# Kernel optimization log

Hardware: AMD Instinct MI355X
Metric: run time of the kernel (lower is better)

## Reference

```python
import jax, jax.numpy as jnp
import numpy as np

B, C, W, H, D = 4, 32, 64, 64, 64


def setup_inputs() -> dict:
    key = jax.random.key(0)
    ks = jax.random.split(key, 8)
    x = jax.random.normal(ks[0], (B, C, W, H, D), dtype=jnp.float32)
    # 1x1x1 Conv3d == per-voxel channel mixing: weight (C_out, C_in), bias (C_out,)
    Wq = jax.random.normal(ks[1], (C, C), dtype=jnp.float32) * 0.05
    bq = jax.random.normal(ks[2], (C,), dtype=jnp.float32) * 0.05
    Wk = jax.random.normal(ks[3], (C, C), dtype=jnp.float32) * 0.05
    bk = jax.random.normal(ks[4], (C,), dtype=jnp.float32) * 0.05
    Wv = jax.random.normal(ks[5], (C, C), dtype=jnp.float32) * 0.05
    bv = jax.random.normal(ks[6], (C,), dtype=jnp.float32) * 0.05
    gamma = jnp.float32(0.1)  # torch inits to 0; nonzero so output depends on attention
    return {"x": x, "Wq": Wq, "bq": bq, "Wk": Wk, "bk": bk, "Wv": Wv, "bv": bv, "gamma": gamma}


def reference(x, Wq, bq, Wk, bk, Wv, bv, gamma):
    b, c, w, h, d = x.shape
    N = w * h * d

    def proj(Wt, bt):
        # 1x1x1 conv then torch's .view(b, -1, c): a raw row-major reshape of
        # (b, c, w, h, d) -> (b, N, c) that interleaves channel/spatial (faithful).
        y = jnp.einsum('oc,bcwhd->bowhd', Wt, x) + bt[None, :, None, None, None]
        return y.reshape(b, N, c)

    q = proj(Wq, bq)  # (b, N, c)
    k = proj(Wk, bk)
    v = proj(Wv, bv)
    s = jnp.einsum('bnc,bnd->bcd', q, k)          # q^T k: tiny (b, c, c)
    a = jax.nn.softmax(s, axis=-1)
    scores = jnp.einsum('bnc,bcd->bnd', v, a)     # (b, N, c)
    return x + gamma * scores.reshape(b, c, w, h, d)
```

## Files before the change

### kernel.cpp

```cpp
#include <hip/hip_runtime.h>

typedef __attribute__((ext_vector_type(8))) short bf16x8;
typedef __attribute__((ext_vector_type(4))) float f32x4;

#define MSP   262144
#define BATCH 4
#define TPOS  256
#define NT1   4
#define NBLK1 (MSP / TPOS / NT1)
#define NBLK2 (MSP / TPOS)

#define OFF_U      0
#define OFF_V      32
#define OFF_BETA   64
#define OFF_CA     96
#define OFF_P      256
#define OFF_CS     4352
#define OFF_UFRAG  8448
#define OFF_WVFRAG 9472
#define OFF_AFRAG  9984

#define GLDS16(gsrc, ldst)                                               \
  __builtin_amdgcn_global_load_lds(                                      \
      (const __attribute__((address_space(1))) unsigned int*)(gsrc),     \
      (__attribute__((address_space(3))) unsigned int*)(ldst), 16, 0, 0)

__device__ __forceinline__ unsigned short f2bf(float f) {
  unsigned int u = __float_as_uint(f);
  u += 0x7fffu + ((u >> 16) & 1u);
  return (unsigned short)(u >> 16);
}
__device__ __forceinline__ float bf2f(unsigned short h) {
  return __uint_as_float(((unsigned int)h) << 16);
}
__device__ __forceinline__ void split2(float f, short* hi, short* lo) {
  unsigned int u = __float_as_uint(f);
  unsigned int uh = u + (0x7fffu + ((u >> 16) & 1u));
  *hi = (short)(uh >> 16);
  const float r = f - __uint_as_float(uh & 0xffff0000u);
  *lo = (short)(__float_as_uint(r) >> 16);
}

#define MFMA(A, B, C) __builtin_amdgcn_mfma_f32_16x16x32_bf16(A, B, C, 0, 0, 0)


__global__ __launch_bounds__(1024) void prep_kernel(
    const float* __restrict__ Wq, const float* __restrict__ bq,
    const float* __restrict__ Wk, const float* __restrict__ bk,
    const float* __restrict__ Wv, float* __restrict__ ws) {
  __shared__ float Ulds[32][32];
  const int tid = threadIdx.x;
  const int aa = tid & 31, bb = tid >> 5;
  float s = 0.f;
  for (int ch = 0; ch < 32; ++ch) s = fmaf(Wq[ch * 32 + aa], Wk[ch * 32 + bb], s);
  Ulds[aa][bb] = s;
  if (tid < 32) {
    float u = 0.f, v = 0.f;
    for (int ch = 0; ch < 32; ++ch) {
      u = fmaf(Wq[ch * 32 + tid], bk[ch], u);
      v = fmaf(bq[ch], Wk[ch * 32 + tid], v);
    }
    ws[OFF_U + tid] = u;
    ws[OFF_V + tid] = v;
  }
  if (tid == 0) {
    float bt = 0.f;
    for (int ch = 0; ch < 32; ++ch) bt = fmaf(bq[ch], bk[ch], bt);
    ws[OFF_BETA] = bt;
  }
  for (int k = tid; k < 8192; k += 1024) ws[OFF_P + k] = 0.f;
  __syncthreads();
  if (tid < 64) {
    const int lm = tid & 15, lb = tid >> 4;
    unsigned short* ufr = (unsigned short*)(ws + OFF_UFRAG);
    unsigned short* wfr = (unsigned short*)(ws + OFF_WVFRAG);
#pragma unroll
    for (int ct = 0; ct < 2; ++ct) {
#pragma unroll
      for (int r = 0; r < 8; ++r) {
        const int kk = (r < 4) ? lb * 4 + r : 16 + lb * 4 + (r - 4);
        const float uval = Ulds[ct * 16 + lm][kk];
        const unsigned short h = f2bf(uval);
        ufr[((ct * 2 + 0) * 64 + tid) * 8 + r] = h;
        ufr[((ct * 2 + 1) * 64 + tid) * 8 + r] = f2bf(uval - bf2f(h));
        wfr[(ct * 64 + tid) * 8 + r] = f2bf(Wv[(ct * 16 + lm) * 32 + kk]);
      }
    }
  }
}

__global__ __launch_bounds__(256) void pass1_kernel(const float* __restrict__ x,
                                                    float* __restrict__ ws) {
  __shared__ float XT[8192];
  const int tid = threadIdx.x;
  const int w = tid >> 6, l = tid & 63, lm = tid & 15, lb = (tid >> 4) & 3;
  const int b = blockIdx.y;
  const size_t xbase = (size_t)b * 32 * MSP;

  const bf16x8* UF = (const bf16x8*)(ws + OFF_UFRAG);
  const bf16x8 uh0 = UF[0 * 64 + l];
  const bf16x8 ul0 = UF[1 * 64 + l];
  const bf16x8 uh1 = UF[2 * 64 + l];
  const bf16x8 ul1 = UF[3 * 64 + l];

  int ldsoff[8];
#pragma unroll
  for (int r = 0; r < 8; ++r) {
    const int ch = (r < 4) ? lb * 4 + r : 16 + lb * 4 + (r - 4);
    ldsoff[r] = ch * 256 + lm;
  }
  const float* rowsrc[8];
#pragma unroll
  for (int rr = 0; rr < 8; ++rr)
    rowsrc[rr] = x + xbase + (size_t)(w * 8 + rr) * MSP + l * 4;

  f32x4 p00 = {0, 0, 0, 0}, p01 = {0, 0, 0, 0}, p10 = {0, 0, 0, 0}, p11 = {0, 0, 0, 0};
  float cs0[8], cs1[8];
#pragma unroll
  for (int r = 0; r < 8; ++r) { cs0[r] = 0.f; cs1[r] = 0.f; }

  const int tile0 = blockIdx.x * NT1;
#pragma unroll 1
  for (int t = 0; t < NT1; ++t) {
    const int pos0 = (tile0 + t) * TPOS;
    __syncthreads();
#pragma unroll
    for (int rr = 0; rr < 8; ++rr)
      GLDS16(rowsrc[rr] + pos0, &XT[(w * 8 + rr) * 256]);
    __syncthreads();

#pragma unroll
    for (int g2 = 0; g2 < 2; ++g2) {
      const int pl = (w * 2 + g2) * 32;
      float xf0[8], xf1[8];
#pragma unroll
      for (int r = 0; r < 8; ++r) {
        xf0[r] = XT[ldsoff[r] + pl];
        xf1[r] = XT[ldsoff[r] + pl + 16];
      }
      bf16x8 xh0, xl0, xh1, xl1;
#pragma unroll
      for (int r = 0; r < 8; ++r) {
        short h, lo;
        split2(xf0[r], &h, &lo); xh0[r] = h; xl0[r] = lo;
        split2(xf1[r], &h, &lo); xh1[r] = h; xl1[r] = lo;
        cs0[r] += xf0[r];  cs1[r] += xf1[r];
      }

      f32x4 y00 = {0,0,0,0}, y01 = {0,0,0,0}, y10 = {0,0,0,0}, y11 = {0,0,0,0};
      y00 = MFMA(uh0, xh0, y00); y00 = MFMA(uh0, xl0, y00); y00 = MFMA(ul0, xh0, y00);
      y01 = MFMA(uh1, xh0, y01); y01 = MFMA(uh1, xl0, y01); y01 = MFMA(ul1, xh0, y01);
      y10 = MFMA(uh0, xh1, y10); y10 = MFMA(uh0, xl1, y10); y10 = MFMA(ul0, xh1, y10);
      y11 = MFMA(uh1, xh1, y11); y11 = MFMA(uh1, xl1, y11); y11 = MFMA(ul1, xh1, y11);

      bf16x8 yh0, yl0, yh1, yl1;
#pragma unroll
      for (int r = 0; r < 4; ++r) {
        short h, lo;
        split2(y00[r], &h, &lo); yh0[r] = h; yl0[r] = lo;
        split2(y10[r], &h, &lo); yh1[r] = h; yl1[r] = lo;
      }
#pragma unroll
      for (int r = 4; r < 8; ++r) {
        short h, lo;
        split2(y01[r - 4], &h, &lo); yh0[r] = h; yl0[r] = lo;
        split2(y11[r - 4], &h, &lo); yh1[r] = h; yl1[r] = lo;
      }

      p00 = MFMA(xh0, yh0, p00); p00 = MFMA(xh0, yl0, p00); p00 = MFMA(xl0, yh0, p00);
      p01 = MFMA(xh0, yh1, p01); p01 = MFMA(xh0, yl1, p01); p01 = MFMA(xl0, yh1, p01);
      p10 = MFMA(xh1, yh0, p10); p10 = MFMA(xh1, yl0, p10); p10 = MFMA(xl1, yh0, p10);
      p11 = MFMA(xh1, yh1, p11); p11 = MFMA(xh1, yl1, p11); p11 = MFMA(xl1, yh1, p11);
    }
  }

  __syncthreads();
  float* red = XT;
#pragma unroll
  for (int r = 0; r < 4; ++r) {
    red[w * 1024 + (lb * 4 + r) * 32 + lm]           = p00[r];
    red[w * 1024 + (lb * 4 + r) * 32 + 16 + lm]      = p01[r];
    red[w * 1024 + (16 + lb * 4 + r) * 32 + lm]      = p10[r];
    red[w * 1024 + (16 + lb * 4 + r) * 32 + 16 + lm] = p11[r];
  }
  __syncthreads();
  for (int k = tid; k < 1024; k += 256) {
    const float s = red[k] + red[1024 + k] + red[2048 + k] + red[3072 + k];
    atomicAdd(&ws[OFF_P + b * 1024 + k], s);
  }
  __syncthreads();
#pragma unroll
  for (int r = 0; r < 8; ++r) {
    const int ch = (r < 4) ? lb * 4 + r : 16 + lb * 4 + (r - 4);
    red[w * 1024 + ch * 32 + lm]      = cs0[r];
    red[w * 1024 + ch * 32 + 16 + lm] = cs1[r];
  }
  __syncthreads();
  for (int k = tid; k < 1024; k += 256) {
    const float s = red[k] + red[1024 + k] + red[2048 + k] + red[3072 + k];
    atomicAdd(&ws[OFF_CS + b * 1024 + k], s);
  }
}

__global__ __launch_bounds__(1024) void softmax_kernel(float* __restrict__ ws) {
  const int j = threadIdx.x, i = threadIdx.y, b = blockIdx.x;
  __shared__ float A_lds[32][32];
  float s = ws[OFF_P + (b * 32 + i) * 32 + j] + 8192.0f * ws[OFF_BETA];
  for (int a = 0; a < 32; ++a) {
    s = fmaf(ws[OFF_U + a], ws[OFF_CS + (b * 32 + a) * 32 + i], s);
    s = fmaf(ws[OFF_V + a], ws[OFF_CS + (b * 32 + a) * 32 + j], s);
  }
  float mx = s;
#pragma unroll
  for (int off = 16; off > 0; off >>= 1) mx = fmaxf(mx, __shfl_xor(mx, off, 32));
  const float e = expf(s - mx);
  float sum = e;
#pragma unroll
  for (int off = 16; off > 0; off >>= 1) sum += __shfl_xor(sum, off, 32);
  A_lds[i][j] = e / sum;
  __syncthreads();
  if (i == 0) {
    float c = 0.f;
    for (int ii = 0; ii < 32; ++ii) c += A_lds[ii][j];
    ws[OFF_CA + b * 32 + j] = c;
  }
  const int tid = i * 32 + j;
  if (tid < 64) {
    const int lm = tid & 15, lb = tid >> 4;
    unsigned short* afr = (unsigned short*)(ws + OFF_AFRAG);
#pragma unroll
    for (int mt = 0; mt < 2; ++mt) {
#pragma unroll
      for (int r = 0; r < 8; ++r) {
        const int kk = (r < 4) ? lb * 4 + r : 16 + lb * 4 + (r - 4);
        afr[((b * 2 + mt) * 64 + tid) * 8 + r] = f2bf(A_lds[kk][mt * 16 + lm]);
      }
    }
  }
}

__global__ __launch_bounds__(256) void pass2_kernel(
    const float* __restrict__ x, const float* __restrict__ bv,
    const float* __restrict__ gm, const float* __restrict__ ws,
    float* __restrict__ out) {
  __shared__ float XT[8192];
  const int tid = threadIdx.x;
  const int w = tid >> 6, l = tid & 63, lm = tid & 15, lb = (tid >> 4) & 3;
  const int b = blockIdx.y;
  const size_t xbase = (size_t)b * 32 * MSP;
  const int pos0 = blockIdx.x * TPOS;

#pragma unroll
  for (int rr = 0; rr < 8; ++rr) {
    const int row = w * 8 + rr;
    const int csrc = ((l + rr) & 63) << 2;
    GLDS16(x + xbase + (size_t)row * MSP + pos0 + csrc, &XT[row * 256]);
  }

  const bf16x8* WF = (const bf16x8*)(ws + OFF_WVFRAG);
  const bf16x8 wv0 = WF[0 * 64 + l];
  const bf16x8 wv1 = WF[1 * 64 + l];
  const bf16x8* AF = (const bf16x8*)(ws + OFF_AFRAG);
  const bf16x8 a0 = AF[(b * 2 + 0) * 64 + l];
  const bf16x8 a1 = AF[(b * 2 + 1) * 64 + l];
  const float gamma = gm[0];
  const float bv0 = bv[lm], bv1 = bv[16 + lm];

  float i00[4], i01[4], i10[4], i11[4];
#pragma unroll
  for (int r = 0; r < 4; ++r) {
    const float c0 = ws[OFF_CA + b * 32 + lb * 4 + r];
    const float c1 = ws[OFF_CA + b * 32 + 16 + lb * 4 + r];
    i00[r] = bv0 * c0; i01[r] = bv1 * c0;
    i10[r] = bv0 * c1; i11[r] = bv1 * c1;
  }

  const int c3 = lm & 3, q = lm >> 2;
  int fbase[8], dr[8];
#pragma unroll
  for (int r = 0; r < 8; ++r) {
    const int ch = (r < 4) ? lb * 4 + r : 16 + lb * 4 + (r - 4);
    fbase[r] = ch * 256 + c3;
    dr[r] = q - (ch & 7);
  }
  const int dres = lb - (lm & 7);
  __syncthreads();

#pragma unroll
  for (int g2 = 0; g2 < 2; ++g2) {
    const int pl4 = (w * 2 + g2) * 8;
    bf16x8 xh0, xh1;
#pragma unroll
    for (int r = 0; r < 8; ++r) {
      const int f0 = fbase[r] + (((pl4 + dr[r]) & 63) << 2);
      const int f1 = fbase[r] + (((pl4 + 4 + dr[r]) & 63) << 2);
      xh0[r] = (short)f2bf(XT[f0]);
      xh1[r] = (short)f2bf(XT[f1]);
    }
    f32x4 v00 = {0,0,0,0}, v01 = {0,0,0,0}, v10 = {0,0,0,0}, v11 = {0,0,0,0};
    v00 = MFMA(xh0, wv0, v00); v01 = MFMA(xh0, wv1, v01);
    v10 = MFMA(xh1, wv0, v10); v11 = MFMA(xh1, wv1, v11);

    bf16x8 vb0, vb1;
#pragma unroll
    for (int r = 0; r < 4; ++r) { vb0[r] = (short)f2bf(v00[r]); vb1[r] = (short)f2bf(v01[r]); }
#pragma unroll
    for (int r = 4; r < 8; ++r) { vb0[r] = (short)f2bf(v10[r - 4]); vb1[r] = (short)f2bf(v11[r - 4]); }

    f32x4 t00 = {i00[0], i00[1], i00[2], i00[3]};
    f32x4 t01 = {i01[0], i01[1], i01[2], i01[3]};
    f32x4 t10 = {i10[0], i10[1], i10[2], i10[3]};
    f32x4 t11 = {i11[0], i11[1], i11[2], i11[3]};
    t00 = MFMA(a0, vb0, t00); t01 = MFMA(a0, vb1, t01);
    t10 = MFMA(a1, vb0, t10); t11 = MFMA(a1, vb1, t11);

    const int p0g = pos0 + (pl4 << 2);
#define EPI(TT, MT, CT)                                                           \
    {                                                                             \
      const int F = ((CT) * 16 + lm) * 256 +                                      \
                    (((pl4 + (MT) * 4 + dres) & 63) << 2);                        \
      const f32x4 xr = *reinterpret_cast<const f32x4*>(&XT[F]);                   \
      const size_t addr = xbase + (size_t)((CT) * 16 + lm) * MSP +                \
                          (size_t)(p0g + (MT) * 16 + lb * 4);                     \
      f32x4 o;                                                                    \
      o[0] = fmaf(gamma, TT[0], xr[0]); o[1] = fmaf(gamma, TT[1], xr[1]);         \
      o[2] = fmaf(gamma, TT[2], xr[2]); o[3] = fmaf(gamma, TT[3], xr[3]);         \
      *reinterpret_cast<f32x4*>(out + addr) = o;                                  \
    }
    EPI(t00, 0, 0); EPI(t01, 0, 1); EPI(t10, 1, 0); EPI(t11, 1, 1);
#undef EPI
  }
}

extern "C" void kernel_launch(void* const* d_in, const int* in_sizes, int n_in,
                              void* d_out, int out_size, void* d_ws, size_t ws_size,
                              hipStream_t stream) {
  const float* x  = (const float*)d_in[0];
  const float* Wq = (const float*)d_in[1];
  const float* bq = (const float*)d_in[2];
  const float* Wk = (const float*)d_in[3];
  const float* bk = (const float*)d_in[4];
  const float* Wv = (const float*)d_in[5];
  const float* bv = (const float*)d_in[6];
  const float* gm = (const float*)d_in[7];
  float* out = (float*)d_out;
  float* ws  = (float*)d_ws;

  prep_kernel<<<1, 1024, 0, stream>>>(Wq, bq, Wk, bk, Wv, ws);
  pass1_kernel<<<dim3(NBLK1, BATCH), 256, 0, stream>>>(x, ws);
  softmax_kernel<<<BATCH, dim3(32, 32), 0, stream>>>(ws);
  pass2_kernel<<<dim3(NBLK2, BATCH), 256, 0, stream>>>(x, bv, gm, ws, out);
}
```

Measured before the change: 97.59 us.

## Fold prep and softmax into passes, double-buffer tile loads, larger per-block tiles

Removes the separate prep and softmax kernels. Each pass1 block now computes Wq^T Wk in LDS, and each pass2 block redundantly recomputes the softmax and bias terms from the workspace sums, with zeroing done by a memset. Both passes now process 8 tiles per block with double-buffered global-to-LDS loads so the next tile's fetch overlaps compute. pass1 pads LDS rows to 258 floats, presumably to reduce bank conflicts. The trade is fewer launches and better latency hiding against redundant per-block setup work, larger LDS use, and fewer blocks in pass2.

Measured after the change: 83.81 us. 1.16x faster.

```diff
diff --git a/kernel.cpp b/kernel.cpp
--- a/kernel.cpp
+++ b/kernel.cpp
@@ -6,19 +6,14 @@
 #define MSP   262144
 #define BATCH 4
 #define TPOS  256
-#define NT1   4
-#define NBLK1 (MSP / TPOS / NT1)
-#define NBLK2 (MSP / TPOS)
-
-#define OFF_U      0
-#define OFF_V      32
-#define OFF_BETA   64
-#define OFF_CA     96
-#define OFF_P      256
-#define OFF_CS     4352
-#define OFF_UFRAG  8448
-#define OFF_WVFRAG 9472
-#define OFF_AFRAG  9984
+#define NT    8
+#define NBLK  (MSP / TPOS / NT)
+
+#define LROW1 258
+#define TSZ1  (32 * LROW1)
+
+#define OFF_P  0
+#define OFF_CS 4096
 
 #define GLDS16(gsrc, ldst)                                               \
   __builtin_amdgcn_global_load_lds(                                      \
@@ -29,9 +24,6 @@
   unsigned int u = __float_as_uint(f);
   u += 0x7fffu + ((u >> 16) & 1u);
   return (unsigned short)(u >> 16);
-}
-__device__ __forceinline__ float bf2f(unsigned short h) {
-  return __uint_as_float(((unsigned int)h) << 16);
 }
 __device__ __forceinline__ void split2(float f, short* hi, short* lo) {
   unsigned int u = __float_as_uint(f);
@@ -44,90 +36,76 @@
 #define MFMA(A, B, C) __builtin_amdgcn_mfma_f32_16x16x32_bf16(A, B, C, 0, 0, 0)
 
 
-__global__ __launch_bounds__(1024) void prep_kernel(
-    const float* __restrict__ Wq, const float* __restrict__ bq,
-    const float* __restrict__ Wk, const float* __restrict__ bk,
-    const float* __restrict__ Wv, float* __restrict__ ws) {
-  __shared__ float Ulds[32][32];
-  const int tid = threadIdx.x;
-  const int aa = tid & 31, bb = tid >> 5;
-  float s = 0.f;
-  for (int ch = 0; ch < 32; ++ch) s = fmaf(Wq[ch * 32 + aa], Wk[ch * 32 + bb], s);
-  Ulds[aa][bb] = s;
-  if (tid < 32) {
-    float u = 0.f, v = 0.f;
-    for (int ch = 0; ch < 32; ++ch) {
-      u = fmaf(Wq[ch * 32 + tid], bk[ch], u);
-      v = fmaf(bq[ch], Wk[ch * 32 + tid], v);
-    }
-    ws[OFF_U + tid] = u;
-    ws[OFF_V + tid] = v;
-  }
-  if (tid == 0) {
-    float bt = 0.f;
-    for (int ch = 0; ch < 32; ++ch) bt = fmaf(bq[ch], bk[ch], bt);
-    ws[OFF_BETA] = bt;
-  }
-  for (int k = tid; k < 8192; k += 1024) ws[OFF_P + k] = 0.f;
-  __syncthreads();
-  if (tid < 64) {
-    const int lm = tid & 15, lb = tid >> 4;
-    unsigned short* ufr = (unsigned short*)(ws + OFF_UFRAG);
-    unsigned short* wfr = (unsigned short*)(ws + OFF_WVFRAG);
-#pragma unroll
-    for (int ct = 0; ct < 2; ++ct) {
-#pragma unroll
-      for (int r = 0; r < 8; ++r) {
-        const int kk = (r < 4) ? lb * 4 + r : 16 + lb * 4 + (r - 4);
-        const float uval = Ulds[ct * 16 + lm][kk];
-        const unsigned short h = f2bf(uval);
-        ufr[((ct * 2 + 0) * 64 + tid) * 8 + r] = h;
-        ufr[((ct * 2 + 1) * 64 + tid) * 8 + r] = f2bf(uval - bf2f(h));
-        wfr[(ct * 64 + tid) * 8 + r] = f2bf(Wv[(ct * 16 + lm) * 32 + kk]);
-      }
-    }
-  }
-}
-
-__global__ __launch_bounds__(256) void pass1_kernel(const float* __restrict__ x,
-                                                    float* __restrict__ ws) {
-  __shared__ float XT[8192];
+__global__ __launch_bounds__(256) void pass1_kernel(
+    const float* __restrict__ x, const float* __restrict__ Wq,
+    const float* __restrict__ Wk, float* __restrict__ ws) {
+  __shared__ float XT[2 * TSZ1];
   const int tid = threadIdx.x;
   const int w = tid >> 6, l = tid & 63, lm = tid & 15, lb = (tid >> 4) & 3;
   const int b = blockIdx.y;
   const size_t xbase = (size_t)b * 32 * MSP;
-
-  const bf16x8* UF = (const bf16x8*)(ws + OFF_UFRAG);
-  const bf16x8 uh0 = UF[0 * 64 + l];
-  const bf16x8 ul0 = UF[1 * 64 + l];
-  const bf16x8 uh1 = UF[2 * 64 + l];
-  const bf16x8 ul1 = UF[3 * 64 + l];
+  const int tile0 = blockIdx.x * NT;
+
+  const float* rowsrc[8];
+#pragma unroll
+  for (int rr = 0; rr < 8; ++rr)
+    rowsrc[rr] = x + xbase + (size_t)(w * 8 + rr) * MSP + l * 4;
+
+#pragma unroll
+  for (int rr = 0; rr < 8; ++rr)
+    GLDS16(rowsrc[rr] + tile0 * TPOS, &XT[(w * 8 + rr) * LROW1]);
+
+  {
+    float* WqL = XT + TSZ1;
+    float* WkL = XT + TSZ1 + 1024;
+    for (int k = tid; k < 1024; k += 256) { WqL[k] = Wq[k]; WkL[k] = Wk[k]; }
+    __syncthreads();
+    float* UL = XT + TSZ1 + 2048;
+    for (int k = tid; k < 1024; k += 256) {
+      const int aa = k >> 5, bb = k & 31;
+      float s = 0.f;
+#pragma unroll
+      for (int ch = 0; ch < 32; ++ch)
+        s = fmaf(WqL[ch * 32 + aa], WkL[ch * 32 + bb], s);
+      UL[k] = s;
+    }
+    __syncthreads();
+  }
+  bf16x8 uh0, ul0, uh1, ul1;
+  {
+    const float* UL = XT + TSZ1 + 2048;
+#pragma unroll
+    for (int r = 0; r < 8; ++r) {
+      const int kk = (r < 4) ? lb * 4 + r : 16 + lb * 4 + (r - 4);
+      short h, lo;
+      split2(UL[lm * 32 + kk], &h, &lo);        uh0[r] = h; ul0[r] = lo;
+      split2(UL[(16 + lm) * 32 + kk], &h, &lo); uh1[r] = h; ul1[r] = lo;
+    }
+  }
+  __syncthreads();
 
   int ldsoff[8];
 #pragma unroll
   for (int r = 0; r < 8; ++r) {
     const int ch = (r < 4) ? lb * 4 + r : 16 + lb * 4 + (r - 4);
-    ldsoff[r] = ch * 256 + lm;
-  }
-  const float* rowsrc[8];
-#pragma unroll
-  for (int rr = 0; rr < 8; ++rr)
-    rowsrc[rr] = x + xbase + (size_t)(w * 8 + rr) * MSP + l * 4;
+    ldsoff[r] = ch * LROW1 + lm;
+  }
 
   f32x4 p00 = {0, 0, 0, 0}, p01 = {0, 0, 0, 0}, p10 = {0, 0, 0, 0}, p11 = {0, 0, 0, 0};
   float cs0[8], cs1[8];
 #pragma unroll
   for (int r = 0; r < 8; ++r) { cs0[r] = 0.f; cs1[r] = 0.f; }
 
-  const int tile0 = blockIdx.x * NT1;
 #pragma unroll 1
-  for (int t = 0; t < NT1; ++t) {
-    const int pos0 = (tile0 + t) * TPOS;
-    __syncthreads();
-#pragma unroll
-    for (int rr = 0; rr < 8; ++rr)
-      GLDS16(rowsrc[rr] + pos0, &XT[(w * 8 + rr) * 256]);
-    __syncthreads();
+  for (int t = 0; t < NT; ++t) {
+    const int cur = t & 1;
+    if (t + 1 < NT) {
+      const int posn = (tile0 + t + 1) * TPOS;
+#pragma unroll
+      for (int rr = 0; rr < 8; ++rr)
+        GLDS16(rowsrc[rr] + posn, &XT[(cur ^ 1) * TSZ1 + (w * 8 + rr) * LROW1]);
+    }
+    const float* XB = XT + cur * TSZ1;
 
 #pragma unroll
     for (int g2 = 0; g2 < 2; ++g2) {
@@ -135,8 +113,8 @@
       float xf0[8], xf1[8];
 #pragma unroll
       for (int r = 0; r < 8; ++r) {
-        xf0[r] = XT[ldsoff[r] + pl];
-        xf1[r] = XT[ldsoff[r] + pl + 16];
+        xf0[r] = XB[ldsoff[r] + pl];
+        xf1[r] = XB[ldsoff[r] + pl + 16];
       }
       bf16x8 xh0, xl0, xh1, xl1;
 #pragma unroll
@@ -172,9 +150,9 @@
       p10 = MFMA(xh1, yh0, p10); p10 = MFMA(xh1, yl0, p10); p10 = MFMA(xl1, yh0, p10);
       p11 = MFMA(xh1, yh1, p11); p11 = MFMA(xh1, yl1, p11); p11 = MFMA(xl1, yh1, p11);
     }
-  }
-
-  __syncthreads();
+    __syncthreads();
+  }
+
   float* red = XT;
 #pragma unroll
   for (int r = 0; r < 4; ++r) {
@@ -202,75 +180,109 @@
   }
 }
 
-__global__ __launch_bounds__(1024) void softmax_kernel(float* __restrict__ ws) {
-  const int j = threadIdx.x, i = threadIdx.y, b = blockIdx.x;
-  __shared__ float A_lds[32][32];
-  float s = ws[OFF_P + (b * 32 + i) * 32 + j] + 8192.0f * ws[OFF_BETA];
-  for (int a = 0; a < 32; ++a) {
-    s = fmaf(ws[OFF_U + a], ws[OFF_CS + (b * 32 + a) * 32 + i], s);
-    s = fmaf(ws[OFF_V + a], ws[OFF_CS + (b * 32 + a) * 32 + j], s);
-  }
-  float mx = s;
-#pragma unroll
-  for (int off = 16; off > 0; off >>= 1) mx = fmaxf(mx, __shfl_xor(mx, off, 32));
-  const float e = expf(s - mx);
-  float sum = e;
-#pragma unroll
-  for (int off = 16; off > 0; off >>= 1) sum += __shfl_xor(sum, off, 32);
-  A_lds[i][j] = e / sum;
-  __syncthreads();
-  if (i == 0) {
-    float c = 0.f;
-    for (int ii = 0; ii < 32; ++ii) c += A_lds[ii][j];
-    ws[OFF_CA + b * 32 + j] = c;
-  }
-  const int tid = i * 32 + j;
-  if (tid < 64) {
-    const int lm = tid & 15, lb = tid >> 4;
-    unsigned short* afr = (unsigned short*)(ws + OFF_AFRAG);
-#pragma unroll
-    for (int mt = 0; mt < 2; ++mt) {
-#pragma unroll
-      for (int r = 0; r < 8; ++r) {
-        const int kk = (r < 4) ? lb * 4 + r : 16 + lb * 4 + (r - 4);
-        afr[((b * 2 + mt) * 64 + tid) * 8 + r] = f2bf(A_lds[kk][mt * 16 + lm]);
-      }
-    }
-  }
-}
-
 __global__ __launch_bounds__(256) void pass2_kernel(
-    const float* __restrict__ x, const float* __restrict__ bv,
-    const float* __restrict__ gm, const float* __restrict__ ws,
-    float* __restrict__ out) {
-  __shared__ float XT[8192];
+    const float* __restrict__ x, const float* __restrict__ Wq,
+    const float* __restrict__ bq, const float* __restrict__ Wk,
+    const float* __restrict__ bk, const float* __restrict__ Wv,
+    const float* __restrict__ bv, const float* __restrict__ gm,
+    const float* __restrict__ ws, float* __restrict__ out) {
+  __shared__ float XT[2 * 8192];
+  __shared__ float Sm[1024];
+  __shared__ float u_l[32], v_l[32], su_l[32], sv_l[32], ca_l[32];
+  __shared__ float beta_l;
+
   const int tid = threadIdx.x;
   const int w = tid >> 6, l = tid & 63, lm = tid & 15, lb = (tid >> 4) & 3;
   const int b = blockIdx.y;
   const size_t xbase = (size_t)b * 32 * MSP;
-  const int pos0 = blockIdx.x * TPOS;
+  const int tile0 = blockIdx.x * NT;
 
 #pragma unroll
   for (int rr = 0; rr < 8; ++rr) {
     const int row = w * 8 + rr;
     const int csrc = ((l + rr) & 63) << 2;
-    GLDS16(x + xbase + (size_t)row * MSP + pos0 + csrc, &XT[row * 256]);
-  }
-
-  const bf16x8* WF = (const bf16x8*)(ws + OFF_WVFRAG);
-  const bf16x8 wv0 = WF[0 * 64 + l];
-  const bf16x8 wv1 = WF[1 * 64 + l];
-  const bf16x8* AF = (const bf16x8*)(ws + OFF_AFRAG);
-  const bf16x8 a0 = AF[(b * 2 + 0) * 64 + l];
-  const bf16x8 a1 = AF[(b * 2 + 1) * 64 + l];
+    GLDS16(x + xbase + (size_t)row * MSP + tile0 * TPOS + csrc, &XT[row * 256]);
+  }
+
+  if (tid < 32) {
+    float u = 0.f;
+#pragma unroll
+    for (int ch = 0; ch < 32; ++ch) u = fmaf(Wq[ch * 32 + tid], bk[ch], u);
+    u_l[tid] = u;
+  } else if (tid < 64) {
+    const int j = tid - 32;
+    float v = 0.f;
+#pragma unroll
+    for (int ch = 0; ch < 32; ++ch) v = fmaf(bq[ch], Wk[ch * 32 + j], v);
+    v_l[j] = v;
+  } else if (tid == 64) {
+    float bt = 0.f;
+#pragma unroll
+    for (int ch = 0; ch < 32; ++ch) bt = fmaf(bq[ch], bk[ch], bt);
+    beta_l = bt;
+  }
+  __syncthreads();
+  if (tid < 32) {
+    float s = 0.f;
+#pragma unroll
+    for (int a = 0; a < 32; ++a)
+      s = fmaf(u_l[a], ws[OFF_CS + b * 1024 + a * 32 + tid], s);
+    su_l[tid] = s;
+  } else if (tid < 64) {
+    const int j = tid - 32;
+    float s = 0.f;
+#pragma unroll
+    for (int a = 0; a < 32; ++a)
+      s = fmaf(v_l[a], ws[OFF_CS + b * 1024 + a * 32 + j], s);
+    sv_l[j] = s;
+  }
+  __syncthreads();
+  {
+    const int si = tid >> 3, sj0 = (tid & 7) * 4;
+    float s4[4];
+#pragma unroll
+    for (int c = 0; c < 4; ++c)
+      s4[c] = ws[OFF_P + b * 1024 + si * 32 + sj0 + c] + su_l[si] +
+              sv_l[sj0 + c] + 8192.0f * beta_l;
+    float mx = fmaxf(fmaxf(s4[0], s4[1]), fmaxf(s4[2], s4[3]));
+    mx = fmaxf(mx, __shfl_xor(mx, 1, 8));
+    mx = fmaxf(mx, __shfl_xor(mx, 2, 8));
+    mx = fmaxf(mx, __shfl_xor(mx, 4, 8));
+    float e4[4], sum = 0.f;
+#pragma unroll
+    for (int c = 0; c < 4; ++c) { e4[c] = expf(s4[c] - mx); sum += e4[c]; }
+    sum += __shfl_xor(sum, 1, 8);
+    sum += __shfl_xor(sum, 2, 8);
+    sum += __shfl_xor(sum, 4, 8);
+    const float inv = 1.0f / sum;
+#pragma unroll
+    for (int c = 0; c < 4; ++c) Sm[si * 32 + sj0 + c] = e4[c] * inv;
+  }
+  __syncthreads();
+  if (tid < 32) {
+    float c = 0.f;
+#pragma unroll
+    for (int ii = 0; ii < 32; ++ii) c += Sm[ii * 32 + tid];
+    ca_l[tid] = c;
+  }
+  bf16x8 a0, a1, wv0, wv1;
+#pragma unroll
+  for (int r = 0; r < 8; ++r) {
+    const int kk = (r < 4) ? lb * 4 + r : 16 + lb * 4 + (r - 4);
+    a0[r]  = (short)f2bf(Sm[kk * 32 + lm]);
+    a1[r]  = (short)f2bf(Sm[kk * 32 + 16 + lm]);
+    wv0[r] = (short)f2bf(Wv[lm * 32 + kk]);
+    wv1[r] = (short)f2bf(Wv[(16 + lm) * 32 + kk]);
+  }
+  __syncthreads();
+
   const float gamma = gm[0];
   const float bv0 = bv[lm], bv1 = bv[16 + lm];
-
   float i00[4], i01[4], i10[4], i11[4];
 #pragma unroll
   for (int r = 0; r < 4; ++r) {
-    const float c0 = ws[OFF_CA + b * 32 + lb * 4 + r];
-    const float c1 = ws[OFF_CA + b * 32 + 16 + lb * 4 + r];
+    const float c0 = ca_l[lb * 4 + r];
+    const float c1 = ca_l[16 + lb * 4 + r];
     i00[r] = bv0 * c0; i01[r] = bv1 * c0;
     i10[r] = bv0 * c1; i11[r] = bv1 * c1;
   }
@@ -284,51 +296,67 @@
     dr[r] = q - (ch & 7);
   }
   const int dres = lb - (lm & 7);
-  __syncthreads();
-
-#pragma unroll
-  for (int g2 = 0; g2 < 2; ++g2) {
-    const int pl4 = (w * 2 + g2) * 8;
-    bf16x8 xh0, xh1;
-#pragma unroll
-    for (int r = 0; r < 8; ++r) {
-      const int f0 = fbase[r] + (((pl4 + dr[r]) & 63) << 2);
-      const int f1 = fbase[r] + (((pl4 + 4 + dr[r]) & 63) << 2);
-      xh0[r] = (short)f2bf(XT[f0]);
-      xh1[r] = (short)f2bf(XT[f1]);
-    }
-    f32x4 v00 = {0,0,0,0}, v01 = {0,0,0,0}, v10 = {0,0,0,0}, v11 = {0,0,0,0};
-    v00 = MFMA(xh0, wv0, v00); v01 = MFMA(xh0, wv1, v01);
-    v10 = MFMA(xh1, wv0, v10); v11 = MFMA(xh1, wv1, v11);
-
-    bf16x8 vb0, vb1;
-#pragma unroll
-    for (int r = 0; r < 4; ++r) { vb0[r] = (short)f2bf(v00[r]); vb1[r] = (short)f2bf(v01[r]); }
-#pragma unroll
-    for (int r = 4; r < 8; ++r) { vb0[r] = (short)f2bf(v10[r - 4]); vb1[r] = (short)f2bf(v11[r - 4]); }
-
-    f32x4 t00 = {i00[0], i00[1], i00[2], i00[3]};
-    f32x4 t01 = {i01[0], i01[1], i01[2], i01[3]};
-    f32x4 t10 = {i10[0], i10[1], i10[2], i10[3]};
-    f32x4 t11 = {i11[0], i11[1], i11[2], i11[3]};
-    t00 = MFMA(a0, vb0, t00); t01 = MFMA(a0, vb1, t01);
-    t10 = MFMA(a1, vb0, t10); t11 = MFMA(a1, vb1, t11);
-
-    const int p0g = pos0 + (pl4 << 2);
+
+#pragma unroll 1
+  for (int t = 0; t < NT; ++t) {
+    const int cur = t & 1;
+    if (t + 1 < NT) {
+      const int posn = (tile0 + t + 1) * TPOS;
+#pragma unroll
+      for (int rr = 0; rr < 8; ++rr) {
+        const int row = w * 8 + rr;
+        const int csrc = ((l + rr) & 63) << 2;
+        GLDS16(x + xbase + (size_t)row * MSP + posn + csrc,
+               &XT[(cur ^ 1) * 8192 + row * 256]);
+      }
+    }
+    const float* XB = XT + cur * 8192;
+    const int pos0 = (tile0 + t) * TPOS;
+
+#pragma unroll
+    for (int g2 = 0; g2 < 2; ++g2) {
+      const int pl4 = (w * 2 + g2) * 8;
+      bf16x8 xh0, xh1;
+#pragma unroll
+      for (int r = 0; r < 8; ++r) {
+        const int f0 = fbase[r] + (((pl4 + dr[r]) & 63) << 2);
+        const int f1 = fbase[r] + (((pl4 + 4 + dr[r]) & 63) << 2);
+        xh0[r] = (short)f2bf(XB[f0]);
+        xh1[r] = (short)f2bf(XB[f1]);
+      }
+      f32x4 v00 = {0,0,0,0}, v01 = {0,0,0,0}, v10 = {0,0,0,0}, v11 = {0,0,0,0};
+      v00 = MFMA(xh0, wv0, v00); v01 = MFMA(xh0, wv1, v01);
+      v10 = MFMA(xh1, wv0, v10); v11 = MFMA(xh1, wv1, v11);
+
+      bf16x8 vb0, vb1;
+#pragma unroll
+      for (int r = 0; r < 4; ++r) { vb0[r] = (short)f2bf(v00[r]); vb1[r] = (short)f2bf(v01[r]); }
+#pragma unroll
+      for (int r = 4; r < 8; ++r) { vb0[r] = (short)f2bf(v10[r - 4]); vb1[r] = (short)f2bf(v11[r - 4]); }
+
+      f32x4 t00 = {i00[0], i00[1], i00[2], i00[3]};
+      f32x4 t01 = {i01[0], i01[1], i01[2], i01[3]};
+      f32x4 t10 = {i10[0], i10[1], i10[2], i10[3]};
+      f32x4 t11 = {i11[0], i11[1], i11[2], i11[3]};
+      t00 = MFMA(a0, vb0, t00); t01 = MFMA(a0, vb1, t01);
+      t10 = MFMA(a1, vb0, t10); t11 = MFMA(a1, vb1, t11);
+
 #define EPI(TT, MT, CT)                                                           \
-    {                                                                             \
-      const int F = ((CT) * 16 + lm) * 256 +                                      \
-                    (((pl4 + (MT) * 4 + dres) & 63) << 2);                        \
-      const f32x4 xr = *reinterpret_cast<const f32x4*>(&XT[F]);                   \
-      const size_t addr = xbase + (size_t)((CT) * 16 + lm) * MSP +                \
-                          (size_t)(p0g + (MT) * 16 + lb * 4);                     \
-      f32x4 o;                                                                    \
-      o[0] = fmaf(gamma, TT[0], xr[0]); o[1] = fmaf(gamma, TT[1], xr[1]);         \
-      o[2] = fmaf(gamma, TT[2], xr[2]); o[3] = fmaf(gamma, TT[3], xr[3]);         \
-      *reinterpret_cast<f32x4*>(out + addr) = o;                                  \
-    }
-    EPI(t00, 0, 0); EPI(t01, 0, 1); EPI(t10, 1, 0); EPI(t11, 1, 1);
+      {                                                                           \
+        const int F = ((CT) * 16 + lm) * 256 +                                    \
+                      (((pl4 + (MT) * 4 + dres) & 63) << 2);                      \
+        const f32x4 xr = *reinterpret_cast<const f32x4*>(&XB[F]);                 \
+        const size_t addr = xbase + (size_t)((CT) * 16 + lm) * MSP +              \
+                            (size_t)(pos0 + (pl4 << 2) + (MT) * 16 + lb * 4);     \
+        f32x4 o;                                                                  \
+        o[0] = fmaf(gamma, TT[0], xr[0]); o[1] = fmaf(gamma, TT[1], xr[1]);       \
+        o[2] = fmaf(gamma, TT[2], xr[2]); o[3] = fmaf(gamma, TT[3], xr[3]);       \
+        *reinterpret_cast<f32x4*>(out + addr) = o;                                \
+      }
+      EPI(t00, 0, 0); EPI(t01, 0, 1); EPI(t10, 1, 0); EPI(t11, 1, 1);
 #undef EPI
+    }
+    __syncthreads();
   }
 }
 
@@ -346,8 +374,8 @@
   float* out = (float*)d_out;
   float* ws  = (float*)d_ws;
 
-  prep_kernel<<<1, 1024, 0, stream>>>(Wq, bq, Wk, bk, Wv, ws);
-  pass1_kernel<<<dim3(NBLK1, BATCH), 256, 0, stream>>>(x, ws);
-  softmax_kernel<<<BATCH, dim3(32, 32), 0, stream>>>(ws);
-  pass2_kernel<<<dim3(NBLK2, BATCH), 256, 0, stream>>>(x, bv, gm, ws, out);
-}
+  hipMemsetAsync(ws, 0, 8192 * sizeof(float), stream);
+  pass1_kernel<<<dim3(NBLK, BATCH), 256, 0, stream>>>(x, Wq, Wk, ws);
+  pass2_kernel<<<dim3(NBLK, BATCH), 256, 0, stream>>>(x, Wq, bq, Wk, bk, Wv, bv,
+                                                      gm, ws, out);
+}
```
